# Optimization experiments

Hardware: AMD Instinct MI355X
Metric: run time of the kernel (lower is better)

The kernel has to match this reference:

```python
import jax, jax.numpy as jnp
import numpy as np

B, S, DIN, PPOS = 2, 128, 768, 256
DCAT = 2 * (DIN + PPOS)   # 2048, BiLSTM input dim
H = DCAT // 2             # 1024, LSTM hidden per direction
MAXLEN = 128              # position embedding table size


def _xavier(k, shape):
    lim = float(np.sqrt(6.0 / (shape[0] + shape[1])))
    return jax.random.uniform(k, shape, jnp.float32, -lim, lim)


def _lstm_u(k, shape):
    lim = float(1.0 / np.sqrt(H))
    return jax.random.uniform(k, shape, jnp.float32, -lim, lim)


def setup_inputs() -> dict:
    key = jax.random.key(0)
    ks = jax.random.split(key, 17)
    inp = {
        "input_embeddings": jax.random.normal(ks[0], (B, S, DIN), jnp.float32),
        "pos_emb": _xavier(ks[1], (MAXLEN, PPOS)),
    }
    i = 2
    for l in (0, 1):
        for d in ("f", "b"):
            inp[f"w_ih_l{l}_{d}"] = _lstm_u(ks[i], (4 * H, DCAT)); i += 1
            inp[f"b_ih_l{l}_{d}"] = _lstm_u(ks[i], (4 * H,)); i += 1
            inp[f"b_hh_l{l}_{d}"] = _lstm_u(ks[i], (4 * H,)); i += 1
    inp["fc_w"] = _lstm_u(ks[i], (1, 2 * H)); i += 1
    inp["fc_b"] = _lstm_u(ks[i], (1,))
    inp["convo_len"] = S
    return inp


def _lstm_dir(x, w_ih, b_ih, b_hh):
    # single timestep, h0=c0=0 -> recurrent term vanishes (grad wrt W_hh is 0)
    g = x @ w_ih.T + b_ih + b_hh            # [N, 4H], pytorch gate order i,f,g,o
    i, f, c, o = jnp.split(g, 4, axis=-1)
    cell = jax.nn.sigmoid(i) * jnp.tanh(c)  # f-gate multiplies c0=0
    return jax.nn.sigmoid(o) * jnp.tanh(cell)


def reference(input_embeddings, pos_emb,
              w_ih_l0_f, b_ih_l0_f, b_hh_l0_f,
              w_ih_l0_b, b_ih_l0_b, b_hh_l0_b,
              w_ih_l1_f, b_ih_l1_f, b_hh_l1_f,
              w_ih_l1_b, b_ih_l1_b, b_hh_l1_b,
              fc_w, fc_b, convo_len):
    # positions indexed by int(norm(embedding)) as in the original code
    idx = jnp.linalg.norm(input_embeddings, axis=-1).astype(jnp.int32)  # [B,S]
    e = jnp.concatenate([input_embeddings, pos_emb[idx]], axis=-1)      # [B,S,D']
    # pair (i,j) -> concat(e_i, e_j)
    left = jnp.repeat(e, S, axis=1)          # [B, S*S, D'], row i repeated S times
    right = jnp.tile(e, (1, S, 1))           # [B, S*S, D'], sequence tiled S times
    p = jnp.concatenate([left, right], axis=-1).reshape(B * S * S, DCAT)
    h1 = jnp.concatenate([
        _lstm_dir(p, w_ih_l0_f, b_ih_l0_f, b_hh_l0_f),
        _lstm_dir(p, w_ih_l0_b, b_ih_l0_b, b_hh_l0_b)], axis=-1)        # [N, 2H]
    h2 = jnp.concatenate([
        _lstm_dir(h1, w_ih_l1_f, b_ih_l1_f, b_hh_l1_f),
        _lstm_dir(h1, w_ih_l1_b, b_ih_l1_b, b_hh_l1_b)], axis=-1)       # [N, 2H]
    logits = h2 @ fc_w.T + fc_b              # [N, 1]
    return logits.reshape(B, S * S)
```

## Files before the change

### kernel.cpp

```cpp
#include <hip/hip_runtime.h>
#include <cstdint>

typedef _Float16 f16;
typedef f16   f16x8 __attribute__((ext_vector_type(8)));
typedef f16   f16x4 __attribute__((ext_vector_type(4)));
typedef float f32x4 __attribute__((ext_vector_type(4)));
typedef float f32x8 __attribute__((ext_vector_type(8)));
typedef int   i32x4 __attribute__((ext_vector_type(4)));
typedef signed char c8x8 __attribute__((ext_vector_type(8)));
typedef unsigned int u32;


static constexpr size_t OFF_E16  = 0;
static constexpr size_t OFF_W0P  = 524288;
static constexpr size_t OFF_UV   = 34078720;
static constexpr size_t OFF_B0   = 50855936;
static constexpr size_t OFF_W1P  = 50888704;
static constexpr size_t OFF_B1   = 76054528;
static constexpr size_t OFF_H1   = 76079104;
static constexpr size_t OFF_PART = 210296832;

__device__ __forceinline__ void gl_lds16(const void* g, void* l) {
  __builtin_amdgcn_global_load_lds((const __attribute__((address_space(1))) u32*)g,
                                   (__attribute__((address_space(3))) u32*)l, 16, 0, 0);
}
__device__ __forceinline__ float sigm(float x) { return 1.f / (1.f + __expf(-x)); }
__device__ __forceinline__ float tanh_f(float x) {
  float e = __expf(-2.f * fabsf(x));
  float t = (1.f - e) / (1.f + e);
  return x < 0.f ? -t : t;
}


__global__ __launch_bounds__(256) void prep_e(const float* __restrict__ x,
                                              const float* __restrict__ pos,
                                              f16* __restrict__ e16) {
  int row = blockIdx.x;
  const float* xr = x + (size_t)row * 768;
  double ss = 0.0;
  for (int i = threadIdx.x; i < 768; i += 256) { float v = xr[i]; ss += (double)v * v; }
  __shared__ double red[256];
  red[threadIdx.x] = ss;
  __syncthreads();
  for (int s2 = 128; s2 > 0; s2 >>= 1) {
    if (threadIdx.x < s2) red[threadIdx.x] += red[threadIdx.x + s2];
    __syncthreads();
  }
  __shared__ int idx_s;
  if (threadIdx.x == 0) {
    int idx = (int)((float)sqrt(red[0]));
    idx_s = idx < 0 ? 0 : (idx > 127 ? 127 : idx);
  }
  __syncthreads();
  int idx = idx_s;
  for (int i = threadIdx.x; i < 1024; i += 256) {
    float v = (i < 768) ? xr[i] : pos[idx * 256 + (i - 768)];
    e16[(size_t)row * 1024 + i] = (f16)v;
  }
}

__global__ __launch_bounds__(256) void prep_w0(const float* __restrict__ w0f,
                                               const float* __restrict__ w0b,
                                               f16* __restrict__ w0p) {
  int t = blockIdx.x * 256 + threadIdx.x;
  int n = t >> 8;
  int k4 = (t & 255) * 4;
  int half = n >> 13;
  int nn = n & 8191;
  int d = nn >> 12;
  int r = nn & 4095;
  const float* w = d ? w0b : w0f;
  float4 v = *(const float4*)(w + (size_t)r * 2048 + half * 1024 + k4);
  f16x4 o;
  o[0] = (f16)v.x; o[1] = (f16)v.y; o[2] = (f16)v.z; o[3] = (f16)v.w;
  *(f16x4*)(w0p + (size_t)n * 1024 + k4) = o;
}

__global__ __launch_bounds__(256) void prep_w1(const float* __restrict__ w1f,
                                               const float* __restrict__ w1b,
                                               signed char* __restrict__ w1q) {
  int t = blockIdx.x * 256 + threadIdx.x;
  int n = t >> 8;
  int c8 = (t & 255) * 8;
  int ct = n / 192, r = n % 192;
  int wn = r / 48, r2 = r % 48;
  int g = r2 >> 4, hs = r2 & 15;
  int d = ct >> 4;
  int h = (ct & 15) * 64 + wn * 16 + hs;
  int gsel = (g == 0) ? 0 : (g + 1);
  const float* w = d ? w1b : w1f;
  const float* src = w + (size_t)(gsel * 1024 + h) * 2048 + c8;
  float4 v0 = *(const float4*)(src);
  float4 v1 = *(const float4*)(src + 4);
  c8x8 o;
  o[0] = (signed char)(int)rintf(v0.x * 4064.f);
  o[1] = (signed char)(int)rintf(v0.y * 4064.f);
  o[2] = (signed char)(int)rintf(v0.z * 4064.f);
  o[3] = (signed char)(int)rintf(v0.w * 4064.f);
  o[4] = (signed char)(int)rintf(v1.x * 4064.f);
  o[5] = (signed char)(int)rintf(v1.y * 4064.f);
  o[6] = (signed char)(int)rintf(v1.z * 4064.f);
  o[7] = (signed char)(int)rintf(v1.w * 4064.f);
  *(c8x8*)(w1q + (size_t)n * 2048 + c8) = o;
}

__global__ void prep_bias(const float* bi0f, const float* bh0f,
                          const float* bi0b, const float* bh0b,
                          const float* bi1f, const float* bh1f,
                          const float* bi1b, const float* bh1b,
                          float* bias0, float* bias1) {
  int i = blockIdx.x * 256 + threadIdx.x;
  if (i < 8192) {
    int d = i >> 12, r = i & 4095;
    bias0[i] = d ? (bi0b[r] + bh0b[r]) : (bi0f[r] + bh0f[r]);
  } else if (i < 8192 + 6144) {
    int n = i - 8192;
    int d = n / 3072, rem = n % 3072;
    int g3 = rem >> 10, k = rem & 1023;
    int gsel = (g3 == 0) ? 0 : (g3 + 1);
    int r = gsel * 1024 + k;
    bias1[n] = d ? (bi1b[r] + bh1b[r]) : (bi1f[r] + bh1f[r]);
  }
}

__global__ __launch_bounds__(256) void gemm_l0(const f16* __restrict__ e16,
                                               const f16* __restrict__ w0p,
                                               float* __restrict__ uv) {
  __shared__ __align__(16) f16 As[8192];
  __shared__ __align__(16) f16 Bs[8192];
  int n0 = blockIdx.x * 128;
  int m0 = blockIdx.y * 128;
  int tid = threadIdx.x, lane = tid & 63, w = tid >> 6;
  int wr = (w >> 1) * 64, wc = (w & 1) * 64;
  f32x4 acc[4][4] = {};

  for (int k0 = 0; k0 < 1024; k0 += 64) {
    __syncthreads();
#pragma unroll
    for (int q = 0; q < 4; q++) {
      int ch = tid + q * 256;
      int c = ch >> 7, r = ch & 127;
      gl_lds16(e16 + (size_t)(m0 + r) * 1024 + k0 + c * 8, (char*)As + ch * 16);
    }
#pragma unroll
    for (int q = 0; q < 4; q++) {
      int ch = tid + q * 256;
      int c = ch >> 7, r = ch & 127;
      gl_lds16(w0p + (size_t)(n0 + r) * 1024 + k0 + c * 8, (char*)Bs + ch * 16);
    }
    __syncthreads();
#pragma unroll
    for (int ks = 0; ks < 2; ks++) {
      int cb = ks * 4 + (lane >> 4);
      f16x8 a[4], b[4];
#pragma unroll
      for (int f = 0; f < 4; f++)
        a[f] = *(const f16x8*)(As + (cb * 128 + wr + f * 16 + (lane & 15)) * 8);
#pragma unroll
      for (int g = 0; g < 4; g++)
        b[g] = *(const f16x8*)(Bs + (cb * 128 + wc + g * 16 + (lane & 15)) * 8);
#pragma unroll
      for (int f = 0; f < 4; f++)
#pragma unroll
        for (int g = 0; g < 4; g++)
          acc[f][g] = __builtin_amdgcn_mfma_f32_16x16x32_f16(a[f], b[g], acc[f][g], 0, 0, 0);
    }
  }
  int col = lane & 15, lg = lane >> 4;
#pragma unroll
  for (int f = 0; f < 4; f++)
#pragma unroll
    for (int g = 0; g < 4; g++)
#pragma unroll
      for (int j = 0; j < 4; j++) {
        int row = m0 + wr + f * 16 + lg * 4 + j;
        int c = n0 + wc + g * 16 + col;
        uv[(size_t)row * 16384 + c] = acc[f][g][j];
      }
}

__global__ __launch_bounds__(256) void pair_h1(const float* __restrict__ uv,
                                               const float* __restrict__ bias0,
                                               signed char* __restrict__ h1q) {
  int row = blockIdx.x;
  int urow = row >> 7;
  int b = row >> 14;
  int vrow = (b << 7) | (row & 127);
  int t = threadIdx.x;
  int u = t * 8;
  int d = u >> 10, k = u & 1023;
  const float* ub = uv + (size_t)urow * 16384 + d * 4096 + k;
  const float* vb = uv + (size_t)vrow * 16384 + 8192 + d * 4096 + k;
  const float* bb = bias0 + d * 4096 + k;
  f32x8 ui = *(const f32x8*)(ub);
  f32x8 uc = *(const f32x8*)(ub + 2048);
  f32x8 uo = *(const f32x8*)(ub + 3072);
  f32x8 vi = *(const f32x8*)(vb);
  f32x8 vc = *(const f32x8*)(vb + 2048);
  f32x8 vo = *(const f32x8*)(vb + 3072);
  f32x8 bi = *(const f32x8*)(bb);
  f32x8 bc = *(const f32x8*)(bb + 2048);
  f32x8 bo = *(const f32x8*)(bb + 3072);
  c8x8 ov;
#pragma unroll
  for (int e = 0; e < 8; e++) {
    float gi = ui[e] + vi[e] + bi[e];
    float gc = uc[e] + vc[e] + bc[e];
    float go = uo[e] + vo[e] + bo[e];
    float cell = sigm(gi) * tanh_f(gc);
    float hv = sigm(go) * tanh_f(cell);
    ov[e] = (signed char)(int)rintf(hv * 127.f);
  }
  *(c8x8*)(h1q + (size_t)row * 2048 + u) = ov;
}

__global__ __launch_bounds__(512, 2) void gemm_l1(const signed char* __restrict__ h1q,
                                                  const signed char* __restrict__ w1q,
                                                  const float* __restrict__ bias1,
                                                  const float* __restrict__ fcw,
                                                  float* __restrict__ partial) {
  __shared__ __align__(16) signed char As[2][32768];
  __shared__ __align__(16) signed char Bs[2][24576];
  int m0 = blockIdx.x * 256;
  int ct = blockIdx.y;
  int d = ct >> 4;
  int tid = threadIdx.x, lane = tid & 63, w = tid >> 6;
  int wm = w >> 2, wn = w & 3;
  int la = lane & 15, lq = lane >> 4, l8 = lane & 7;

  const signed char* asrc[4]; signed char* adst[4];
#pragma unroll
  for (int q = 0; q < 4; q++) {
    int ch = tid + q * 512, r = ch >> 3, slot = ch & 7, c = slot ^ (r & 7);
    asrc[q] = h1q + (size_t)(m0 + r) * 2048 + c * 16;
    adst[q] = &As[0][ch * 16];
  }
  const signed char* bsrc[3]; signed char* bdst[3];
#pragma unroll
  for (int q = 0; q < 3; q++) {
    int ch = tid + q * 512, pr = ch >> 3, slot = ch & 7, c = slot ^ (pr & 7);
    bsrc[q] = w1q + (size_t)(ct * 192 + pr) * 2048 + c * 16;
    bdst[q] = &Bs[0][ch * 16];
  }
  auto stageA = [&](int t, int b) {
#pragma unroll
    for (int q = 0; q < 4; q++) gl_lds16(asrc[q] + t * 128, adst[q] + b * 32768);
  };
  auto stageB = [&](int t, int b) {
#pragma unroll
    for (int q = 0; q < 3; q++) gl_lds16(bsrc[q] + t * 128, bdst[q] + b * 24576);
  };

  i32x4 acc[8][3] = {};
  stageA(0, 0); stageB(0, 0);
  asm volatile("s_waitcnt vmcnt(0)" ::: "memory");
  __builtin_amdgcn_s_barrier();

  for (int t = 0; t < 16; ++t) {
    int b = t & 1;
    const signed char* Ab = &As[b][0];
    const signed char* Bb = &Bs[b][0];
    i32x4 bf[2][3];
#pragma unroll
    for (int p = 0; p < 4; p++) {
      i32x4 a[2][2];
#pragma unroll
      for (int ks = 0; ks < 2; ks++) {
        int slot = (ks * 4 + lq) ^ l8;
#pragma unroll
        for (int rq = 0; rq < 2; rq++) {
          int R = wm * 128 + (p * 2 + rq) * 16 + la;
          a[ks][rq] = *(const i32x4*)(Ab + (R * 8 + slot) * 16);
        }
        if (p == 0) {
#pragma unroll
          for (int cf = 0; cf < 3; cf++) {
            int P = wn * 48 + cf * 16 + la;
            bf[ks][cf] = *(const i32x4*)(Bb + (P * 8 + slot) * 16);
          }
        }
      }
      if (t < 15) {
        if (p == 0) stageA(t + 1, b ^ 1);
        else if (p == 1) stageB(t + 1, b ^ 1);
      }
      __builtin_amdgcn_s_barrier();
      asm volatile("s_waitcnt lgkmcnt(0)" ::: "memory");
      __builtin_amdgcn_sched_barrier(0);
      __builtin_amdgcn_s_setprio(1);
#pragma unroll
      for (int ks = 0; ks < 2; ks++)
#pragma unroll
        for (int rq = 0; rq < 2; rq++)
#pragma unroll
          for (int cf = 0; cf < 3; cf++)
            acc[p * 2 + rq][cf] = __builtin_amdgcn_mfma_i32_16x16x64_i8(
                a[ks][rq], bf[ks][cf], acc[p * 2 + rq][cf], 0, 0, 0);
      __builtin_amdgcn_s_setprio(0);
      if (p == 3 && t < 15) { asm volatile("s_waitcnt vmcnt(0)" ::: "memory"); }
      __builtin_amdgcn_s_barrier();
    }
  }

  float* sred = (float*)&As[0][0];
  const float S = 1.0f / 516128.0f;
  int hcol = (ct & 15) * 64 + wn * 16 + la;
  float bi = bias1[(d * 3 + 0) * 1024 + hcol];
  float bc = bias1[(d * 3 + 1) * 1024 + hcol];
  float bo = bias1[(d * 3 + 2) * 1024 + hcol];
  float wf = fcw[d * 1024 + hcol];
#pragma unroll
  for (int rf = 0; rf < 8; rf++) {
#pragma unroll
    for (int j = 0; j < 4; j++) {
      float gi = (float)acc[rf][0][j] * S + bi;
      float gc = (float)acc[rf][1][j] * S + bc;
      float go = (float)acc[rf][2][j] * S + bo;
      float cell = sigm(gi) * tanh_f(gc);
      float hv = sigm(go) * tanh_f(cell);
      float v = hv * wf;
      v += __shfl_xor(v, 1);
      v += __shfl_xor(v, 2);
      v += __shfl_xor(v, 4);
      v += __shfl_xor(v, 8);
      if (la == 0) sred[wn * 256 + wm * 128 + rf * 16 + lq * 4 + j] = v;
    }
  }
  __syncthreads();
  if (tid < 256) {
    float s = sred[tid] + sred[256 + tid] + sred[512 + tid] + sred[768 + tid];
    partial[(size_t)ct * 32768 + m0 + tid] = s;
  }
}

__global__ void reduce_out(const float* __restrict__ partial,
                           const float* __restrict__ fcb,
                           float* __restrict__ out) {
  int m = blockIdx.x * 256 + threadIdx.x;
  float s = fcb[0];
#pragma unroll
  for (int ct = 0; ct < 32; ct++) s += partial[(size_t)ct * 32768 + m];
  out[m] = s;
}

extern "C" void kernel_launch(void* const* d_in, const int* in_sizes, int n_in,
                              void* d_out, int out_size, void* d_ws, size_t ws_size,
                              hipStream_t stream) {
  const float* x    = (const float*)d_in[0];
  const float* pos  = (const float*)d_in[1];
  const float* w0f  = (const float*)d_in[2];
  const float* bi0f = (const float*)d_in[3];
  const float* bh0f = (const float*)d_in[4];
  const float* w0b  = (const float*)d_in[5];
  const float* bi0b = (const float*)d_in[6];
  const float* bh0b = (const float*)d_in[7];
  const float* w1f  = (const float*)d_in[8];
  const float* bi1f = (const float*)d_in[9];
  const float* bh1f = (const float*)d_in[10];
  const float* w1b  = (const float*)d_in[11];
  const float* bi1b = (const float*)d_in[12];
  const float* bh1b = (const float*)d_in[13];
  const float* fcw  = (const float*)d_in[14];
  const float* fcb  = (const float*)d_in[15];
  float* out = (float*)d_out;

  char* ws = (char*)d_ws;
  f16*   e16   = (f16*)(ws + OFF_E16);
  f16*   w0p   = (f16*)(ws + OFF_W0P);
  float* uv    = (float*)(ws + OFF_UV);
  float* bias0 = (float*)(ws + OFF_B0);
  signed char* w1q = (signed char*)(ws + OFF_W1P);
  float* bias1 = (float*)(ws + OFF_B1);
  signed char* h1q = (signed char*)(ws + OFF_H1);
  float* part  = (float*)(ws + OFF_PART);

  prep_e<<<256, 256, 0, stream>>>(x, pos, e16);
  prep_w0<<<16384, 256, 0, stream>>>(w0f, w0b, w0p);
  prep_w1<<<6144, 256, 0, stream>>>(w1f, w1b, w1q);
  prep_bias<<<56, 256, 0, stream>>>(bi0f, bh0f, bi0b, bh0b, bi1f, bh1f, bi1b, bh1b,
                                    bias0, bias1);
  gemm_l0<<<dim3(128, 2), 256, 0, stream>>>(e16, w0p, uv);
  pair_h1<<<32768, 256, 0, stream>>>(uv, bias0, h1q);
  gemm_l1<<<dim3(128, 32), 512, 0, stream>>>(h1q, w1q, bias1, fcw, part);
  reduce_out<<<128, 256, 0, stream>>>(part, fcb, out);
}
```

Before: 795.0 us.

## Restructure layer-1 int8 GEMM pipeline with triple-buffered B and full-tile fragment loads

Reworks the gemm_l1 main loop so each K step loads all A and B fragments from LDS at once, issues the next A tile and the B tile two steps ahead, then runs all MFMAs with a single barrier per step instead of four phases. B staging grows to three LDS buffers with partial vmcnt waits, occupancy is lowered to one block per CU via launch bounds, and the grid is transposed so consecutive blocks share the same A rows across column tiles. The goal is fewer barriers and better latency hiding, at the cost of more registers for fragments and lower occupancy.

```diff
diff --git a/kernel.cpp b/kernel.cpp
--- a/kernel.cpp
+++ b/kernel.cpp
@@ -214,15 +214,15 @@
   *(c8x8*)(h1q + (size_t)row * 2048 + u) = ov;
 }
 
-__global__ __launch_bounds__(512, 2) void gemm_l1(const signed char* __restrict__ h1q,
+__global__ __launch_bounds__(512, 1) void gemm_l1(const signed char* __restrict__ h1q,
                                                   const signed char* __restrict__ w1q,
                                                   const float* __restrict__ bias1,
                                                   const float* __restrict__ fcw,
                                                   float* __restrict__ partial) {
   __shared__ __align__(16) signed char As[2][32768];
-  __shared__ __align__(16) signed char Bs[2][24576];
-  int m0 = blockIdx.x * 256;
-  int ct = blockIdx.y;
+  __shared__ __align__(16) signed char Bs[3][24576];
+  int ct = blockIdx.x;
+  int m0 = blockIdx.y * 256;
   int d = ct >> 4;
   int tid = threadIdx.x, lane = tid & 63, w = tid >> 6;
   int wm = w >> 2, wn = w & 3;
@@ -242,67 +242,59 @@
     bsrc[q] = w1q + (size_t)(ct * 192 + pr) * 2048 + c * 16;
     bdst[q] = &Bs[0][ch * 16];
   }
-  auto stageA = [&](int t, int b) {
-#pragma unroll
-    for (int q = 0; q < 4; q++) gl_lds16(asrc[q] + t * 128, adst[q] + b * 32768);
+  auto stageA = [&](int t, int ab) {
+#pragma unroll
+    for (int q = 0; q < 4; q++) gl_lds16(asrc[q] + t * 128, adst[q] + ab * 32768);
   };
-  auto stageB = [&](int t, int b) {
-#pragma unroll
-    for (int q = 0; q < 3; q++) gl_lds16(bsrc[q] + t * 128, bdst[q] + b * 24576);
+  auto stageB = [&](int t, int bb) {
+#pragma unroll
+    for (int q = 0; q < 3; q++) gl_lds16(bsrc[q] + t * 128, bdst[q] + bb * 24576);
   };
 
   i32x4 acc[8][3] = {};
-  stageA(0, 0); stageB(0, 0);
-  asm volatile("s_waitcnt vmcnt(0)" ::: "memory");
+  stageA(0, 0); stageB(0, 0); stageB(1, 1);
+  asm volatile("s_waitcnt vmcnt(3)" ::: "memory");
   __builtin_amdgcn_s_barrier();
 
   for (int t = 0; t < 16; ++t) {
-    int b = t & 1;
-    const signed char* Ab = &As[b][0];
-    const signed char* Bb = &Bs[b][0];
-    i32x4 bf[2][3];
-#pragma unroll
-    for (int p = 0; p < 4; p++) {
-      i32x4 a[2][2];
-#pragma unroll
-      for (int ks = 0; ks < 2; ks++) {
-        int slot = (ks * 4 + lq) ^ l8;
-#pragma unroll
-        for (int rq = 0; rq < 2; rq++) {
-          int R = wm * 128 + (p * 2 + rq) * 16 + la;
-          a[ks][rq] = *(const i32x4*)(Ab + (R * 8 + slot) * 16);
-        }
-        if (p == 0) {
-#pragma unroll
-          for (int cf = 0; cf < 3; cf++) {
-            int P = wn * 48 + cf * 16 + la;
-            bf[ks][cf] = *(const i32x4*)(Bb + (P * 8 + slot) * 16);
-          }
-        }
+    int ab = t & 1;
+    int bb = t % 3;
+    const signed char* Ab = &As[ab][0];
+    const signed char* Bb = &Bs[bb][0];
+    i32x4 af[2][8], bf[2][3];
+#pragma unroll
+    for (int ks = 0; ks < 2; ks++) {
+      int slot = (ks * 4 + lq) ^ l8;
+#pragma unroll
+      for (int rf = 0; rf < 8; rf++) {
+        int R = wm * 128 + rf * 16 + la;
+        af[ks][rf] = *(const i32x4*)(Ab + (R * 8 + slot) * 16);
       }
-      if (t < 15) {
-        if (p == 0) stageA(t + 1, b ^ 1);
-        else if (p == 1) stageB(t + 1, b ^ 1);
+#pragma unroll
+      for (int cf = 0; cf < 3; cf++) {
+        int P = wn * 48 + cf * 16 + la;
+        bf[ks][cf] = *(const i32x4*)(Bb + (P * 8 + slot) * 16);
       }
-      __builtin_amdgcn_s_barrier();
-      asm volatile("s_waitcnt lgkmcnt(0)" ::: "memory");
-      __builtin_amdgcn_sched_barrier(0);
-      __builtin_amdgcn_s_setprio(1);
-#pragma unroll
-      for (int ks = 0; ks < 2; ks++)
-#pragma unroll
-        for (int rq = 0; rq < 2; rq++)
-#pragma unroll
-          for (int cf = 0; cf < 3; cf++)
-            acc[p * 2 + rq][cf] = __builtin_amdgcn_mfma_i32_16x16x64_i8(
-                a[ks][rq], bf[ks][cf], acc[p * 2 + rq][cf], 0, 0, 0);
-      __builtin_amdgcn_s_setprio(0);
-      if (p == 3 && t < 15) { asm volatile("s_waitcnt vmcnt(0)" ::: "memory"); }
-      __builtin_amdgcn_s_barrier();
-    }
-  }
-
-  float* sred = (float*)&As[0][0];
+    }
+    if (t < 15) stageA(t + 1, (t + 1) & 1);
+    if (t < 14) stageB(t + 2, (t + 2) % 3);
+    __builtin_amdgcn_s_setprio(1);
+#pragma unroll
+    for (int ks = 0; ks < 2; ks++)
+#pragma unroll
+      for (int rf = 0; rf < 8; rf++)
+#pragma unroll
+        for (int cf = 0; cf < 3; cf++)
+          acc[rf][cf] = __builtin_amdgcn_mfma_i32_16x16x64_i8(
+              af[ks][rf], bf[ks][cf], acc[rf][cf], 0, 0, 0);
+    __builtin_amdgcn_s_setprio(0);
+    if (t < 14)      { asm volatile("s_waitcnt vmcnt(3)" ::: "memory"); }
+    else             { asm volatile("s_waitcnt vmcnt(0)" ::: "memory"); }
+    __builtin_amdgcn_sched_barrier(0);
+    __builtin_amdgcn_s_barrier();
+  }
+
+  float* sred = (float*)&Bs[0][0];
   const float S = 1.0f / 516128.0f;
   int hcol = (ct & 15) * 64 + wn * 16 + la;
   float bi = bias1[(d * 3 + 0) * 1024 + hcol];
@@ -381,6 +373,6 @@
                                     bias0, bias1);
   gemm_l0<<<dim3(128, 2), 256, 0, stream>>>(e16, w0p, uv);
   pair_h1<<<32768, 256, 0, stream>>>(uv, bias0, h1q);
-  gemm_l1<<<dim3(128, 32), 512, 0, stream>>>(h1q, w1q, bias1, fcw, part);
+  gemm_l1<<<dim3(32, 128), 512, 0, stream>>>(h1q, w1q, bias1, fcw, part);
   reduce_out<<<128, 256, 0, stream>>>(part, fcb, out);
 }
```

After: 696.4 us. -12.4%, faster.
